# Performance work log

Measured on AMD Instinct MI355X. Metric: run time of the kernel, lower is better.

## Reference

```python
import jax, jax.numpy as jnp
import numpy as np

B, S, K, N = 4, 2048, 4096, 4096


def setup_inputs() -> dict:
    key = jax.random.key(0)
    kx, kw = jax.random.split(key)
    # int8 activations and weights in [-127, 127), matching torch.randint(-127,127,...)
    x = jax.random.randint(kx, (B, S, K), -127, 127, dtype=jnp.int32).astype(jnp.int8)
    weight = jax.random.randint(kw, (N, K), -127, 127, dtype=jnp.int32).astype(jnp.int8)
    bias = jnp.zeros((1, N), dtype=jnp.int32)
    out_scale = jnp.ones((), dtype=jnp.float32)
    bias_scale = jnp.ones((), dtype=jnp.float32)
    return {"x": x, "weight": weight, "bias": bias,
            "out_scale": out_scale, "bias_scale": bias_scale}


def reference(x, weight, bias, out_scale, bias_scale):
    # Flatten leading dims: [B, S, K] -> [M, K]
    x_shape = x.shape
    x2 = x.reshape(-1, x_shape[-1])
    acc = jax.lax.dot_general(
        x2, weight,
        dimension_numbers=(((1,), (1,)), ((), ())),
        preferred_element_type=jnp.int32,
    )  # [M, N] int32
    # Fused epilogue: y = round(out_scale * acc + bias_scale * bias) -> int32
    y = jnp.round(acc.astype(jnp.float32) * out_scale
                  + bias.astype(jnp.float32) * bias_scale).astype(jnp.int32)
    return y.reshape(*x_shape[:-1], -1)
```

## Files before the change

### kernel.cpp

```cpp
#include <hip/hip_runtime.h>
#include <stdint.h>


typedef int v4i __attribute__((ext_vector_type(4)));

#define BM 256
#define BN 256
#define BK 128
#define KK 4096
#define KT (KK / BK)

__global__ __launch_bounds__(256)
void pack_i32_to_i8(const v4i* __restrict__ src, int* __restrict__ dst, int n4) {
    int i = blockIdx.x * blockDim.x + threadIdx.x;
    if (i >= n4) return;
    v4i a = src[i];
    dst[i] = (a[0] & 0xff) | ((a[1] & 0xff) << 8) | ((a[2] & 0xff) << 16) | (a[3] << 24);
}

__device__ __forceinline__ void gld_lds16(const void* g, void* lds) {
    __builtin_amdgcn_global_load_lds(
        (const __attribute__((address_space(1))) unsigned int*)g,
        (__attribute__((address_space(3))) unsigned int*)lds,
        16, 0, 0);
}

#define MFMA_I8 __builtin_amdgcn_mfma_i32_16x16x64_i8

__global__ __launch_bounds__(512, 2)
void w8a8_gemm_kernel(const int8_t* __restrict__ X,
                      const int8_t* __restrict__ W,
                      const int*    __restrict__ bias,
                      const float*  __restrict__ out_scale_p,
                      const float*  __restrict__ bias_scale_p,
                      int*          __restrict__ Y,
                      int M, int N)
{
    __shared__ __align__(16) int8_t sA[2 * BM * BK];
    __shared__ __align__(16) int8_t sB[2 * BN * BK];

    const int tid = threadIdx.x;

    const int nbx = N / BN;
    const int nby = M / BM;
    int bx, by;
    {
        const int wg = blockIdx.x;
        if (nbx == 16 && nby == 32) {
            const int x = wg & 7;
            const int k = wg >> 3;
            bx = ((x & 1) << 3) | (k & 7);
            by = ((x >> 1) << 3) | (k >> 3);
        } else { bx = wg % nbx; by = wg / nbx; }
    }
    const int bn = bx * BN;
    const int bm = by * BM;

    const float out_scale  = *out_scale_p;
    const float bias_scale = *bias_scale_p;

    const int8_t* Abase = X + (size_t)bm * KK;
    const int8_t* Bbase = W + (size_t)bn * KK;

    const int r0  = tid >> 3;
    const int j0  = tid & 7;
    const int sw  = (j0 ^ (r0 & 7)) << 4;
    const size_t gOff = (size_t)r0 * KK + sw;
    const int  lOff = tid << 4;

#define STAGE(gbase, lds, t, h) do {                                              \
        const int8_t* _g = (gbase) + (size_t)((h) * 128) * KK                     \
                                   + (size_t)(t) * BK + gOff;                     \
        int8_t* _l = (lds) + (((t) & 1) << 15) + ((h) << 14) + lOff;              \
        gld_lds16(_g,                  _l);                                       \
        gld_lds16(_g + (size_t)64 * KK, _l + 8192);                               \
    } while (0)

    const int w    = tid >> 6;
    const int l    = tid & 63;
    const int wmw  = w >> 2;
    const int wnw  = w & 3;
    const int tm   = l & 15;
    const int quad = l >> 4;
    const int s3   = tm & 7;
    const int xo0  = ( quad      ^ s3) << 4;
    const int xo1  = ((quad + 4) ^ s3) << 4;
    const int rowA = ((wmw << 7) + tm) << 7;
    const int rowB = ((wnw << 6) + tm) << 7;

    v4i acc[8][4];
    const v4i vz = {0, 0, 0, 0};
#pragma unroll
    for (int i = 0; i < 8; ++i)
#pragma unroll
        for (int j = 0; j < 4; ++j)
            acc[i][j] = vz;

    STAGE(Abase, sA, 0, 0); STAGE(Abase, sA, 0, 1);
    STAGE(Bbase, sB, 0, 0); STAGE(Bbase, sB, 0, 1);
    __syncthreads();

#pragma unroll 2
    for (int t = 0; t < KT; ++t) {
        const int bo = (t & 1) << 15;
        const int8_t* sAb = sA + bo;
        const int8_t* sBb = sB + bo;

        if (t + 1 < KT) {
            STAGE(Abase, sA, t + 1, 0); STAGE(Abase, sA, t + 1, 1);
            STAGE(Bbase, sB, t + 1, 0); STAGE(Bbase, sB, t + 1, 1);
        }
        __builtin_amdgcn_sched_barrier(0);

        v4i a[8], b[4];
#pragma unroll
        for (int i = 0; i < 8; ++i)
            a[i] = *(const v4i*)(sAb + rowA + i * 2048 + xo0);
#pragma unroll
        for (int j = 0; j < 4; ++j)
            b[j] = *(const v4i*)(sBb + rowB + j * 2048 + xo0);
#pragma unroll
        for (int i = 0; i < 8; ++i)
#pragma unroll
            for (int j = 0; j < 4; ++j)
                acc[i][j] = MFMA_I8(a[i], b[j], acc[i][j], 0, 0, 0);
#pragma unroll
        for (int i = 0; i < 8; ++i)
            a[i] = *(const v4i*)(sAb + rowA + i * 2048 + xo1);
#pragma unroll
        for (int j = 0; j < 4; ++j)
            b[j] = *(const v4i*)(sBb + rowB + j * 2048 + xo1);
#pragma unroll
        for (int i = 0; i < 8; ++i)
#pragma unroll
            for (int j = 0; j < 4; ++j)
                acc[i][j] = MFMA_I8(a[i], b[j], acc[i][j], 0, 0, 0);

        __syncthreads();
    }
#undef STAGE

    float bb[4];
#pragma unroll
    for (int j = 0; j < 4; ++j)
        bb[j] = (float)bias[bn + (wnw << 6) + (j << 4) + tm] * bias_scale;
#pragma unroll
    for (int i = 0; i < 8; ++i) {
        const int mb = bm + (wmw << 7) + (i << 4) + (quad << 2);
#pragma unroll
        for (int r = 0; r < 4; ++r) {
            int* yrow = Y + (size_t)(mb + r) * N + bn + (wnw << 6) + tm;
#pragma unroll
            for (int j = 0; j < 4; ++j) {
                const float v = (float)acc[i][j][r] * out_scale + bb[j];
                yrow[j << 4] = (int)rintf(v);
            }
        }
    }
}

extern "C" void kernel_launch(void* const* d_in, const int* in_sizes, int n_in,
                              void* d_out, int out_size, void* d_ws, size_t ws_size,
                              hipStream_t stream) {
    const int* x32 = (const int*)d_in[0];
    const int* w32 = (const int*)d_in[1];
    const int*    bias = (const int*)d_in[2];
    const float*  os   = (const float*)d_in[3];
    const float*  bs   = (const float*)d_in[4];
    int* out = (int*)d_out;

    const int K = KK;
    const int M = in_sizes[0] / K;
    const int N = in_sizes[1] / K;
    const int nx = in_sizes[0];
    const int nw = in_sizes[1];

    int8_t* x8 = (int8_t*)d_ws;
    int8_t* w8 = x8 + (size_t)nx;

    pack_i32_to_i8<<<dim3(nx / 4 / 256), dim3(256), 0, stream>>>((const v4i*)x32, (int*)x8, nx / 4);
    pack_i32_to_i8<<<dim3(nw / 4 / 256), dim3(256), 0, stream>>>((const v4i*)w32, (int*)w8, nw / 4);

    dim3 grid((N / BN) * (M / BM));
    dim3 block(512);
    hipLaunchKernelGGL(w8a8_gemm_kernel, grid, block, 0, stream,
                       x8, w8, bias, os, bs, out, M, N);
}
```

Baseline: 396.3 us.

## Double-buffer LDS fragments in registers and prefetch global tiles two ahead

The main loop is restructured so both K-halves of the next tile's A/B fragments are read from LDS into a second register set while MFMAs run on the current set. Global-to-LDS staging now runs two tiles ahead and is issued after the fragment reads. Each iteration has a single barrier, placed between the two MFMA halves. This is meant to hide LDS read latency behind MFMA work, at the cost of roughly 24 extra 128-bit registers per thread, which may cause spills or lower occupancy under the 512x2 launch bound.

```diff
diff --git a/kernel.cpp b/kernel.cpp
--- a/kernel.cpp
+++ b/kernel.cpp
@@ -26,6 +26,7 @@
 }
 
 #define MFMA_I8 __builtin_amdgcn_mfma_i32_16x16x64_i8
+#define SB0()   __builtin_amdgcn_sched_barrier(0)
 
 __global__ __launch_bounds__(512, 2)
 void w8a8_gemm_kernel(const int8_t* __restrict__ X,
@@ -96,47 +97,70 @@
         for (int j = 0; j < 4; ++j)
             acc[i][j] = vz;
 
+    v4i a0[8], b0[4];
+    v4i a1[8], b1[4];
+
     STAGE(Abase, sA, 0, 0); STAGE(Abase, sA, 0, 1);
     STAGE(Bbase, sB, 0, 0); STAGE(Bbase, sB, 0, 1);
     __syncthreads();
+#pragma unroll
+    for (int i = 0; i < 8; ++i) {
+        a0[i] = *(const v4i*)(sA + rowA + i * 2048 + xo0);
+        a1[i] = *(const v4i*)(sA + rowA + i * 2048 + xo1);
+    }
+#pragma unroll
+    for (int j = 0; j < 4; ++j) {
+        b0[j] = *(const v4i*)(sB + rowB + j * 2048 + xo0);
+        b1[j] = *(const v4i*)(sB + rowB + j * 2048 + xo1);
+    }
+    STAGE(Abase, sA, 1, 0); STAGE(Abase, sA, 1, 1);
+    STAGE(Bbase, sB, 1, 0); STAGE(Bbase, sB, 1, 1);
+    SB0();
 
 #pragma unroll 2
     for (int t = 0; t < KT; ++t) {
-        const int bo = (t & 1) << 15;
-        const int8_t* sAb = sA + bo;
-        const int8_t* sBb = sB + bo;
+        const int bo1 = ((t + 1) & 1) << 15;
+        const int8_t* sA1 = sA + bo1;
+        const int8_t* sB1 = sB + bo1;
+
+#pragma unroll
+        for (int i = 0; i < 8; ++i)
+#pragma unroll
+            for (int j = 0; j < 4; ++j)
+                acc[i][j] = MFMA_I8(a0[i], b0[j], acc[i][j], 0, 0, 0);
+        SB0();
+        __syncthreads();
 
         if (t + 1 < KT) {
-            STAGE(Abase, sA, t + 1, 0); STAGE(Abase, sA, t + 1, 1);
-            STAGE(Bbase, sB, t + 1, 0); STAGE(Bbase, sB, t + 1, 1);
-        }
-        __builtin_amdgcn_sched_barrier(0);
-
-        v4i a[8], b[4];
+#pragma unroll
+            for (int i = 0; i < 8; ++i)
+                a0[i] = *(const v4i*)(sA1 + rowA + i * 2048 + xo0);
+#pragma unroll
+            for (int j = 0; j < 4; ++j)
+                b0[j] = *(const v4i*)(sB1 + rowB + j * 2048 + xo0);
+        }
+        SB0();
+
 #pragma unroll
         for (int i = 0; i < 8; ++i)
-            a[i] = *(const v4i*)(sAb + rowA + i * 2048 + xo0);
-#pragma unroll
-        for (int j = 0; j < 4; ++j)
-            b[j] = *(const v4i*)(sBb + rowB + j * 2048 + xo0);
-#pragma unroll
-        for (int i = 0; i < 8; ++i)
-#pragma unroll
-            for (int j = 0; j < 4; ++j)
-                acc[i][j] = MFMA_I8(a[i], b[j], acc[i][j], 0, 0, 0);
-#pragma unroll
-        for (int i = 0; i < 8; ++i)
-            a[i] = *(const v4i*)(sAb + rowA + i * 2048 + xo1);
-#pragma unroll
-        for (int j = 0; j < 4; ++j)
-            b[j] = *(const v4i*)(sBb + rowB + j * 2048 + xo1);
-#pragma unroll
-        for (int i = 0; i < 8; ++i)
-#pragma unroll
-            for (int j = 0; j < 4; ++j)
-                acc[i][j] = MFMA_I8(a[i], b[j], acc[i][j], 0, 0, 0);
-
-        __syncthreads();
+#pragma unroll
+            for (int j = 0; j < 4; ++j)
+                acc[i][j] = MFMA_I8(a1[i], b1[j], acc[i][j], 0, 0, 0);
+
+        if (t + 1 < KT) {
+#pragma unroll
+            for (int i = 0; i < 8; ++i)
+                a1[i] = *(const v4i*)(sA1 + rowA + i * 2048 + xo1);
+#pragma unroll
+            for (int j = 0; j < 4; ++j)
+                b1[j] = *(const v4i*)(sB1 + rowB + j * 2048 + xo1);
+        }
+
+        if (t + 2 < KT) {
+            STAGE(Abase, sA, t + 2, 0); STAGE(Abase, sA, t + 2, 1);
+            STAGE(Bbase, sB, t + 2, 0); STAGE(Bbase, sB, t + 2, 1);
+        }
+        SB0();
     }
 #undef STAGE
 
```

Measured after the change: 676.8 us. 70.8% more time.
